# Kernel tuning notes

Measured on AMD Instinct MI355X. Metric: run time of the kernel, lower is better.

## Reference

```python
import jax, jax.numpy as jnp
import numpy as np
from jax import lax


def setup_inputs() -> dict:
    key = jax.random.key(0)
    k1, k2 = jax.random.split(key)
    B, C = 128, 256
    z_f = jax.random.normal(k1, (B, C, 7, 7), dtype=jnp.float32)
    x_f = jax.random.normal(k2, (B, C, 31, 31), dtype=jnp.float32)
    return {"z_f": z_f, "x_f": x_f}


def xcorr_depthwise(search, kernel):
    # search: [B, C, Hx, Wx], kernel: [B, C, Hz, Wz]
    B, C, Hx, Wx = search.shape
    _, _, Hz, Wz = kernel.shape
    s = search.reshape(1, B * C, Hx, Wx)          # [1, B*C, Hx, Wx]
    k = kernel.reshape(B * C, 1, Hz, Wz)          # [B*C, 1, Hz, Wz]
    out = lax.conv_general_dilated(
        s, k,
        window_strides=(1, 1),
        padding='VALID',
        dimension_numbers=('NCHW', 'OIHW', 'NCHW'),
        feature_group_count=B * C,
    )                                             # [1, B*C, Ho, Wo]
    Ho, Wo = Hx - Hz + 1, Wx - Wz + 1
    return out.reshape(B, C, Ho, Wo)


def reference(z_f, x_f):
    # DepthwiseRPN.forward: xcorr_depthwise(search=x_f, kernel=z_f)
    return xcorr_depthwise(x_f, z_f)
```

## Files before the change

kernel.cpp:

```cpp
#include <hip/hip_runtime.h>


#define PPB 10
#define WX 31
#define XPLANE 961
#define TDW (PPB * XPLANE)
#define XREG 9616
#define ZPLANE 49
#define ZDW (PPB * ZPLANE)
#define ZREG 496
#define OPLANE 625
#define WO 25

typedef __attribute__((address_space(1))) const void gaddr_t;
typedef __attribute__((address_space(3))) void laddr_t;

__global__ __launch_bounds__(256) void dwxcorr_kernel(
    const float* __restrict__ z, const float* __restrict__ x,
    float* __restrict__ out, int nplanes, int ntiles) {
  __shared__ float lds[XREG + ZREG];

  const int tid = threadIdx.x;
  const int t = blockIdx.x;
  const int wb4 = (tid & ~63) * 4;
  const long XTOT = (long)nplanes * XPLANE;
  const long ZTOT = (long)nplanes * ZPLANE;

  const long xoff = (long)t * TDW;
  const long g0 = xoff & ~3L;
  const int off0 = (int)(xoff & 3);
  const long zoff = (long)t * ZDW;
  const long gz0 = zoff & ~3L;
  const int offz = (int)(zoff & 3);

  if (g0 + XREG <= XTOT && gz0 + ZREG <= ZTOT) {
#pragma unroll
    for (int c = 0; c < 9; ++c)
      __builtin_amdgcn_global_load_lds((gaddr_t*)(x + g0 + c * 1024 + tid * 4),
                                       (laddr_t*)&lds[c * 1024 + wb4], 16, 0, 0);
    if (tid < 100)
      __builtin_amdgcn_global_load_lds((gaddr_t*)(x + g0 + 9216 + tid * 4),
                                       (laddr_t*)&lds[9216 + wb4], 16, 0, 0);
    if (tid < 124)
      __builtin_amdgcn_global_load_lds((gaddr_t*)(z + gz0 + tid * 4),
                                       (laddr_t*)&lds[XREG + wb4], 16, 0, 0);
  } else {
#pragma unroll
    for (int c = 0; c < 9; ++c) {
      long gd = g0 + c * 1024 + tid * 4;
      if (gd > XTOT - 4) gd = XTOT - 4;
      __builtin_amdgcn_global_load_lds((gaddr_t*)(x + gd),
                                       (laddr_t*)&lds[c * 1024 + wb4], 16, 0, 0);
    }
    if (tid < 100) {
      long gd = g0 + 9216 + tid * 4;
      if (gd > XTOT - 4) gd = XTOT - 4;
      __builtin_amdgcn_global_load_lds((gaddr_t*)(x + gd),
                                       (laddr_t*)&lds[9216 + wb4], 16, 0, 0);
    }
    if (tid < 124) {
      long gd = gz0 + tid * 4;
      if (gd > ZTOT - 4) gd = ZTOT - 4;
      __builtin_amdgcn_global_load_lds((gaddr_t*)(z + gd),
                                       (laddr_t*)&lds[XREG + wb4], 16, 0, 0);
    }
  }
  __syncthreads();

  const int p0 = t * PPB;
  const int pmax = min(PPB, nplanes - p0);
  const int cpp = tid / 25;
  if (tid >= PPB * 25 || cpp >= pmax) return;
  const int t25 = tid - cpp * 25;
  const int ty = t25 / 5;
  const int tx = t25 - ty * 5;
  const int tx5 = tx * 5;

  const float* zb = &lds[XREG + offz + cpp * ZPLANE];
  float zr[ZPLANE];
#pragma unroll
  for (int j = 0; j < ZPLANE; ++j) zr[j] = zb[j];

  float acc[5][5];
#pragma unroll
  for (int r = 0; r < 5; ++r)
#pragma unroll
    for (int j = 0; j < 5; ++j) acc[r][j] = 0.0f;

  const float* pb = &lds[off0 + cpp * XPLANE + (ty * 5) * WX + tx5];

#pragma unroll
  for (int iy = 0; iy < 11; ++iy) {
    float xr[11];
#pragma unroll
    for (int k = 0; k < 11; ++k) xr[k] = pb[iy * WX + k];
    const int ky_lo = (iy - 4 < 0) ? 0 : iy - 4;
    const int ky_hi = (iy < 6) ? iy : 6;
#pragma unroll
    for (int ky = 0; ky < 7; ++ky) {
      if (ky < ky_lo || ky > ky_hi) continue;
      const int orow = iy - ky;
#pragma unroll
      for (int kx = 0; kx < 7; ++kx) {
        const float zv = zr[ky * 7 + kx];
#pragma unroll
        for (int j = 0; j < 5; ++j)
          acc[orow][j] = fmaf(xr[kx + j], zv, acc[orow][j]);
      }
    }
  }

  float* ob = out + (long)(p0 + cpp) * OPLANE + (ty * 5) * WO + tx5;
#pragma unroll
  for (int r = 0; r < 5; ++r)
#pragma unroll
    for (int j = 0; j < 5; ++j) ob[r * WO + j] = acc[r][j];
}

extern "C" void kernel_launch(void* const* d_in, const int* in_sizes, int n_in,
                              void* d_out, int out_size, void* d_ws, size_t ws_size,
                              hipStream_t stream) {
  const float* z = (const float*)d_in[0];
  const float* x = (const float*)d_in[1];
  float* out = (float*)d_out;

  const int nplanes = in_sizes[0] / ZPLANE;
  const int ntiles = (nplanes + PPB - 1) / PPB;

  hipLaunchKernelGGL(dwxcorr_kernel, dim3(ntiles), dim3(256), 0, stream,
                     z, x, out, nplanes, ntiles);
}
```

Before: 47.99 us.

## Swizzle padded LDS plane layout and halve planes per block

Each 31x31 search plane is now stored in LDS as 32-float rows, with an XOR swizzle on the column index keyed by row. This is meant to avoid the bank conflicts of unaligned 31-stride row reads when threads load their 11-wide windows. The block also shrinks from 10 planes and 256 threads to 5 planes and 128 threads, which cuts LDS use per block so more blocks can be resident. The cost is more complex address arithmetic, unaligned 16-byte global loads for the fast path, and a tail path of scalar 4-byte loads.

Result: faster. 45.47 us (-5.2%).

```diff
diff --git a/kernel.cpp b/kernel.cpp
--- a/kernel.cpp
+++ b/kernel.cpp
@@ -1,67 +1,69 @@
 #include <hip/hip_runtime.h>
 
 
-#define PPB 10
+#define PPB 5
 #define WX 31
 #define XPLANE 961
 #define TDW (PPB * XPLANE)
-#define XREG 9616
+#define LPLANE 1024
+#define XREG (PPB * LPLANE)
 #define ZPLANE 49
 #define ZDW (PPB * ZPLANE)
-#define ZREG 496
+#define ZREG 256
 #define OPLANE 625
 #define WO 25
 
 typedef __attribute__((address_space(1))) const void gaddr_t;
 typedef __attribute__((address_space(3))) void laddr_t;
 
-__global__ __launch_bounds__(256) void dwxcorr_kernel(
+__global__ __launch_bounds__(128, 2) void dwxcorr_kernel(
     const float* __restrict__ z, const float* __restrict__ x,
-    float* __restrict__ out, int nplanes, int ntiles) {
+    float* __restrict__ out, int nplanes) {
   __shared__ float lds[XREG + ZREG];
 
   const int tid = threadIdx.x;
   const int t = blockIdx.x;
   const int wb4 = (tid & ~63) * 4;
+  const int wb1 = tid & ~63;
   const long XTOT = (long)nplanes * XPLANE;
   const long ZTOT = (long)nplanes * ZPLANE;
-
   const long xoff = (long)t * TDW;
-  const long g0 = xoff & ~3L;
-  const int off0 = (int)(xoff & 3);
   const long zoff = (long)t * ZDW;
   const long gz0 = zoff & ~3L;
   const int offz = (int)(zoff & 3);
 
-  if (g0 + XREG <= XTOT && gz0 + ZREG <= ZTOT) {
+  if (xoff + TDW + 31 <= XTOT && gz0 + ZREG <= ZTOT) {
 #pragma unroll
-    for (int c = 0; c < 9; ++c)
-      __builtin_amdgcn_global_load_lds((gaddr_t*)(x + g0 + c * 1024 + tid * 4),
-                                       (laddr_t*)&lds[c * 1024 + wb4], 16, 0, 0);
-    if (tid < 100)
-      __builtin_amdgcn_global_load_lds((gaddr_t*)(x + g0 + 9216 + tid * 4),
-                                       (laddr_t*)&lds[9216 + wb4], 16, 0, 0);
-    if (tid < 124)
+    for (int c = 0; c < 10; ++c) {
+      int s = c * 512 + tid * 4;
+      int p = s >> 10;
+      int row = (s >> 5) & 31;
+      int q = s & 31;
+      int qq = q ^ ((row & 7) << 2);
+      long g = xoff + p * XPLANE + row * WX + qq;
+      __builtin_amdgcn_global_load_lds((gaddr_t*)(x + g),
+                                       (laddr_t*)&lds[c * 512 + wb4], 16, 0, 0);
+    }
+    if (tid < 63)
       __builtin_amdgcn_global_load_lds((gaddr_t*)(z + gz0 + tid * 4),
                                        (laddr_t*)&lds[XREG + wb4], 16, 0, 0);
   } else {
 #pragma unroll
-    for (int c = 0; c < 9; ++c) {
-      long gd = g0 + c * 1024 + tid * 4;
-      if (gd > XTOT - 4) gd = XTOT - 4;
-      __builtin_amdgcn_global_load_lds((gaddr_t*)(x + gd),
-                                       (laddr_t*)&lds[c * 1024 + wb4], 16, 0, 0);
+    for (int c = 0; c < 40; ++c) {
+      int s = c * 128 + tid;
+      int p = s >> 10;
+      int row = (s >> 5) & 31;
+      int q = s & 31;
+      int qq = q ^ ((row & 7) << 2);
+      long g = xoff + p * XPLANE + row * WX + qq;
+      if (g > XTOT - 1) g = XTOT - 1;
+      __builtin_amdgcn_global_load_lds((gaddr_t*)(x + g),
+                                       (laddr_t*)&lds[c * 128 + wb1], 4, 0, 0);
     }
-    if (tid < 100) {
-      long gd = g0 + 9216 + tid * 4;
-      if (gd > XTOT - 4) gd = XTOT - 4;
-      __builtin_amdgcn_global_load_lds((gaddr_t*)(x + gd),
-                                       (laddr_t*)&lds[9216 + wb4], 16, 0, 0);
-    }
-    if (tid < 124) {
-      long gd = gz0 + tid * 4;
-      if (gd > ZTOT - 4) gd = ZTOT - 4;
-      __builtin_amdgcn_global_load_lds((gaddr_t*)(z + gd),
+    if (tid < 63) {
+      long gz = gz0 + tid * 4;
+      if (gz > ZTOT - 4) gz = ZTOT - 4;
+      __builtin_amdgcn_global_load_lds((gaddr_t*)(z + gz),
                                        (laddr_t*)&lds[XREG + wb4], 16, 0, 0);
     }
   }
@@ -87,13 +89,16 @@
 #pragma unroll
     for (int j = 0; j < 5; ++j) acc[r][j] = 0.0f;
 
-  const float* pb = &lds[off0 + cpp * XPLANE + (ty * 5) * WX + tx5];
+  const float* pb = &lds[cpp * LPLANE];
 
 #pragma unroll
   for (int iy = 0; iy < 11; ++iy) {
+    const int row = ty * 5 + iy;
+    const int rb = row << 5;
+    const int f = (row & 7) << 2;
     float xr[11];
 #pragma unroll
-    for (int k = 0; k < 11; ++k) xr[k] = pb[iy * WX + k];
+    for (int k = 0; k < 11; ++k) xr[k] = pb[rb + ((tx5 + k) ^ f)];
     const int ky_lo = (iy - 4 < 0) ? 0 : iy - 4;
     const int ky_hi = (iy < 6) ? iy : 6;
 #pragma unroll
@@ -125,8 +130,8 @@
   float* out = (float*)d_out;
 
   const int nplanes = in_sizes[0] / ZPLANE;
-  const int ntiles = (nplanes + PPB - 1) / PPB;
+  const int blocks = (nplanes + PPB - 1) / PPB;
 
-  hipLaunchKernelGGL(dwxcorr_kernel, dim3(ntiles), dim3(256), 0, stream,
-                     z, x, out, nplanes, ntiles);
+  hipLaunchKernelGGL(dwxcorr_kernel, dim3(blocks), dim3(128), 0, stream,
+                     z, x, out, nplanes);
 }
```
